# Kernel optimization log

Hardware: AMD Instinct MI355X
Metric: run time of the kernel (lower is better)

Reference implementation:

```python
import jax, jax.numpy as jnp
import numpy as np

BS, N_LINKS, MAX_LEN = 8192, 512, 32
D_LINK, D_PATH, D_READ, N_OUT = 32, 128, 256, 3
BN_EPS = 1e-5


def setup_inputs() -> dict:
    key = jax.random.key(0)
    ks = jax.random.split(key, 16)
    capa = jax.random.uniform(ks[0], (BS, N_LINKS), jnp.float32, 0.5, 1.0) * 100.0
    avail = jax.random.uniform(ks[1], (BS, N_LINKS), jnp.float32) * capa
    loss = jax.random.uniform(ks[2], (BS, N_LINKS), jnp.float32) * 0.05
    demand = jax.random.uniform(ks[3], (BS,), jnp.float32) * 10.0
    path = jax.random.randint(ks[4], (BS, MAX_LEN), 0, N_LINKS)
    hop_num = jax.random.randint(ks[5], (BS,), 1, MAX_LEN + 1)
    s = 0.1
    inp = {
        "demand": demand,
        "link_avail_capacity": avail,
        "link_capacity": capa,
        "link_loss": loss,
        "path": path,
        "hop_num": hop_num,
        # GRU params (PyTorch layout: [3H, D] gates ordered r,z,n)
        "gru_w_ih": jax.random.normal(ks[6], (3 * D_PATH, D_LINK), jnp.float32) * s,
        "gru_w_hh": jax.random.normal(ks[7], (3 * D_PATH, D_PATH), jnp.float32) * s,
        "gru_b_ih": jax.random.normal(ks[8], (3 * D_PATH,), jnp.float32) * s,
        "gru_b_hh": jax.random.normal(ks[9], (3 * D_PATH,), jnp.float32) * s,
        "bn_gamma": jnp.ones((D_PATH,), jnp.float32),
        "bn_beta": jnp.zeros((D_PATH,), jnp.float32),
        # stacked readout heads [N_OUT, ...]
        "rW1": jax.random.normal(ks[10], (N_OUT, D_PATH, D_READ), jnp.float32) * s,
        "rb1": jnp.zeros((N_OUT, D_READ), jnp.float32),
        "rW2": jax.random.normal(ks[11], (N_OUT, D_READ, D_READ), jnp.float32) * s,
        "rb2": jnp.zeros((N_OUT, D_READ), jnp.float32),
        "rW3": jax.random.normal(ks[12], (N_OUT, D_READ, 1), jnp.float32) * s,
        "rb3": jnp.zeros((N_OUT, 1), jnp.float32),
    }
    return inp


def _gru_scan(x_bt, h0, w_ih, w_hh, b_ih, b_hh):
    # x_bt: [B, T, D]; h0: [B, H] -> outputs [B, T, H]
    H = h0.shape[-1]
    def step(h, x_t):
        gi = x_t @ w_ih.T + b_ih          # [B, 3H]
        gh = h @ w_hh.T + b_hh            # [B, 3H]
        i_r, i_z, i_n = gi[:, :H], gi[:, H:2*H], gi[:, 2*H:]
        h_r, h_z, h_n = gh[:, :H], gh[:, H:2*H], gh[:, 2*H:]
        r = jax.nn.sigmoid(i_r + h_r)
        z = jax.nn.sigmoid(i_z + h_z)
        n = jnp.tanh(i_n + r * h_n)
        h_new = (1.0 - z) * n + z * h
        return h_new, h_new
    _, outs = jax.lax.scan(step, h0, jnp.swapaxes(x_bt, 0, 1))
    return jnp.swapaxes(outs, 0, 1)


def reference(demand, link_avail_capacity, link_capacity, link_loss, path, hop_num,
              gru_w_ih, gru_w_hh, gru_b_ih, gru_b_hh, bn_gamma, bn_beta,
              rW1, rb1, rW2, rb2, rW3, rb3):
    bs, n_links = link_capacity.shape
    max_len = path.shape[1]
    max_capa = jax.lax.stop_gradient(jnp.max(link_capacity))
    # link_state: [B, n_links, D_LINK]; first D_LINK-4 channels are zeros
    feats = jnp.stack([
        link_avail_capacity / max_capa,
        link_capacity / max_capa,
        link_avail_capacity / link_capacity,
        link_loss,
    ], axis=-1)
    link_state = jnp.concatenate(
        [jnp.zeros((bs, n_links, D_LINK - 4), feats.dtype), feats], axis=-1)
    link_state = jax.lax.stop_gradient(link_state)  # original detaches
    # initial hidden: zeros except last channel = demand/max_capa
    h0 = jnp.concatenate(
        [jnp.zeros((bs, D_PATH - 1), feats.dtype), (demand / max_capa)[:, None]], axis=-1)
    # fused gather of link states along each path, masked past hop_num
    gathered = jnp.take_along_axis(link_state, path[:, :, None], axis=1)  # [B, T, D]
    mask = (jnp.arange(max_len)[None, :] < hop_num[:, None])[:, :, None]
    link_inputs = gathered * mask.astype(gathered.dtype)
    outputs = _gru_scan(link_inputs, h0, gru_w_ih, gru_w_hh, gru_b_ih, gru_b_hh)
    # extract hidden state at last hop of each path
    idx = (hop_num - 1)[:, None, None]
    flow = jnp.take_along_axis(outputs, idx, axis=1)[:, 0, :]  # [B, H]
    # BatchNorm1d (training mode: batch statistics, biased variance)
    mean = jnp.mean(flow, axis=0)
    var = jnp.mean((flow - mean) ** 2, axis=0)
    flow = (flow - mean) * jax.lax.rsqrt(var + BN_EPS) * bn_gamma + bn_beta
    # readout heads: Linear -> SELU -> Linear -> SELU -> Linear
    h1 = jax.nn.selu(jnp.einsum('bh,uhr->ubr', flow, rW1) + rb1[:, None, :])
    h2 = jax.nn.selu(jnp.einsum('ubr,urs->ubs', h1, rW2) + rb2[:, None, :])
    y = jnp.einsum('ubs,uso->ubo', h2, rW3) + rb3[:, None, :]  # [U, B, 1]
    return jnp.transpose(y[:, :, 0], (1, 0))  # [B, U]
```

## Files before the change

kernel.cpp:

```cpp
#include <hip/hip_runtime.h>


#define BS 8192
#define NL 512
#define ML 32
#define DP 128
#define DR 256
#define NJOB 512

#define OFF_SUM    64
#define OFF_SSQ    192
#define OFF_CUR    576
#define OFF_PERM   640
#define OFF_WHH16  (OFF_PERM + BS)
#define OFF_W1     (OFF_WHH16 + 24576)
#define OFF_W2     (OFF_W1 + 49152)
#define OFF_FEATS  (OFF_W2 + 98304)
#define OFF_FLOW   (OFF_FEATS + BS*ML*4)

#define FEATS_BLOCKS 1024
#define MAX_BLOCKS   256
#define WPREP_BLOCKS 1344
#define SORT_BID     (FEATS_BLOCKS + MAX_BLOCKS + WPREP_BLOCKS)
#define PREP_GRID    (SORT_BID + 1)

typedef _Float16 f16x8 __attribute__((ext_vector_type(8)));
typedef float    f32x4 __attribute__((ext_vector_type(4)));

__device__ __forceinline__ float sigmoidf_(float x){ return 1.0f/(1.0f+__expf(-x)); }
__device__ __forceinline__ float tanhf_(float x){
  float t = __expf(-2.0f*fabsf(x));
  float r = (1.0f-t)/(1.0f+t);
  return copysignf(r, x);
}
__device__ __forceinline__ float seluf_(float x){
  const float sc = 1.0507009873554805f, al = 1.6732632423543772f;
  return x > 0.0f ? sc*x : sc*al*(__expf(x)-1.0f);
}

__global__ void prep_all(const int* __restrict__ path, const int* __restrict__ hop,
                         const float* __restrict__ avail, const float* __restrict__ capa,
                         const float* __restrict__ loss, const float* __restrict__ whh,
                         const float* __restrict__ rW1, const float* __restrict__ rW2,
                         float* ws){
  const int bid = blockIdx.x;
  const int tid = threadIdx.x;

  if (bid < FEATS_BLOCKS){
    int idx = bid*256 + tid;
    int b = idx >> 5, t = idx & 31;
    float4 f = make_float4(0.f, 0.f, 0.f, 0.f);
    if (t < hop[b]){
      int l = path[idx];
      float a = avail[b*NL + l];
      float c = capa [b*NL + l];
      f.x = a; f.y = c; f.z = a / c; f.w = loss[b*NL + l];
    }
    ((float4*)(ws + OFF_FEATS))[idx] = f;
  } else if (bid < FEATS_BLOCKS + MAX_BLOCKS){
    const float4* c4 = (const float4*)capa;
    const int n4 = BS*NL/4;
    float m = 0.0f;
    for (int i = (bid - FEATS_BLOCKS)*256 + tid; i < n4; i += MAX_BLOCKS*256){
      float4 v = c4[i];
      m = fmaxf(m, fmaxf(fmaxf(v.x, v.y), fmaxf(v.z, v.w)));
    }
    #pragma unroll
    for (int o = 32; o > 0; o >>= 1) m = fmaxf(m, __shfl_down(m, o, 64));
    if ((tid & 63) == 0) atomicMax((int*)ws, __float_as_int(m));
  } else if (bid < SORT_BID){
    _Float16* whh16 = (_Float16*)(ws + OFF_WHH16);
    _Float16* w1    = (_Float16*)(ws + OFF_W1);
    _Float16* w2    = (_Float16*)(ws + OFF_W2);
    int i = (bid - FEATS_BLOCKS - MAX_BLOCKS)*256 + tid;
    if (i < 49152){
      whh16[i] = (_Float16)whh[i];
    } else if (i < 147456){
      int j = i - 49152; int u = j >> 15; int rem = j & 32767; int n = rem >> 7; int k = rem & 127;
      w1[j] = (_Float16)rW1[u*32768 + k*256 + n];
    } else if (i < 344064){
      int j = i - 147456; int u = j >> 16; int rem = j & 65535; int n = rem >> 8; int k = rem & 255;
      w2[j] = (_Float16)rW2[u*65536 + k*256 + n];
    }
  } else {
    __shared__ int hist[32], start[32];
    for (int i = 64 + tid; i < 640; i += 256) ws[i] = 0.0f;
    if (tid < 32) hist[tid] = 0;
    __syncthreads();
    for (int b = tid; b < BS; b += 256) atomicAdd(&hist[32 - hop[b]], 1);
    __syncthreads();
    if (tid == 0){ int acc = 0; for (int i = 0; i < 32; ++i){ start[i] = acc; acc += hist[i]; } }
    __syncthreads();
    int* perm = (int*)ws + OFF_PERM;
    for (int b = tid; b < BS; b += 256){
      int pos = atomicAdd(&start[32 - hop[b]], 1);
      perm[pos] = b;
    }
  }
}

__launch_bounds__(512, 3)
__global__ void kgru(const float* __restrict__ demand, const int* __restrict__ hop,
                     const float* __restrict__ wih, const float* __restrict__ bih,
                     const float* __restrict__ bhh, float* __restrict__ ws,
                     float* __restrict__ flow){
  __shared__ _Float16 hHI[2][16*136];
  __shared__ _Float16 hLO[2][16*136];
  __shared__ int s_q;
  const int tid  = threadIdx.x;
  const int w    = tid >> 6;
  const int lane = tid & 63;
  const int lm   = lane & 15;
  const int qd   = lane >> 4;
  const int ch   = w*16 + lm;
  const float inv_maxc = 1.0f / ws[0];
  const int* perm = (const int*)ws + OFF_PERM;
  int* cursor = (int*)ws + OFF_CUR;
  const float* feats = ws + OFF_FEATS;
  const _Float16* whh16 = (const _Float16*)(ws + OFF_WHH16);

  f16x8 bf[3][4];
  #pragma unroll
  for (int g = 0; g < 3; ++g){
    const int n = 128*g + ch;
    #pragma unroll
    for (int kc = 0; kc < 4; ++kc)
      bf[g][kc] = *(const f16x8*)(whh16 + n*128 + kc*32 + qd*8);
  }

  float wihc[3][4];
  #pragma unroll
  for (int g = 0; g < 3; ++g){
    #pragma unroll
    for (int c = 0; c < 4; ++c)
      wihc[g][c] = wih[(128*g + ch)*32 + 28 + c];
    wihc[g][0] *= inv_maxc;
    wihc[g][1] *= inv_maxc;
  }
  const float bR  = bih[ch]     + bhh[ch];
  const float bZ  = bih[128+ch] + bhh[128+ch];
  const float bNI = bih[256+ch];
  const float bNH = bhh[256+ch];

  float ssum = 0.f, ssq = 0.f;

  for (;;){
    if (tid == 0) s_q = atomicAdd(cursor, 1);
    __syncthreads();
    const int q = s_q;
    if (q >= NJOB) break;

    int it[4], hp[4];
    #pragma unroll
    for (int r = 0; r < 4; ++r){
      it[r] = perm[q*16 + qd*4 + r];
      hp[r] = hop[it[r]];
    }
    int tmax = max(max(hp[0],hp[1]), max(hp[2],hp[3]));
    tmax = max(tmax, __shfl_xor(tmax, 16, 64));
    tmax = max(tmax, __shfl_xor(tmax, 32, 64));

    float hprev[4];
    #pragma unroll
    for (int r = 0; r < 4; ++r){
      float h0 = (ch == 127) ? demand[it[r]] * inv_maxc : 0.0f;
      hprev[r] = h0;
      const int m = qd*4 + r;
      _Float16 hi = (_Float16)h0;
      hHI[0][m*136 + ch] = hi;
      hLO[0][m*136 + ch] = (_Float16)(h0 - (float)hi);
    }
    __syncthreads();

    for (int t = 0; t < tmax; ++t){
      const int cur = t & 1, nxt = cur ^ 1;
      f32x4 ft[4];
      #pragma unroll
      for (int r = 0; r < 4; ++r)
        ft[r] = *(const f32x4*)(feats + (it[r]*ML + t)*4);

      f16x8 ahi[4], alo[4];
      #pragma unroll
      for (int kc = 0; kc < 4; ++kc){
        const int off = lm*136 + kc*32 + qd*8;
        ahi[kc] = *(const f16x8*)(&hHI[cur][off]);
        alo[kc] = *(const f16x8*)(&hLO[cur][off]);
      }

      f32x4 acc[3];
      #pragma unroll
      for (int g = 0; g < 3; ++g){
        f32x4 a = {0.f, 0.f, 0.f, 0.f};
        #pragma unroll
        for (int kc = 0; kc < 4; ++kc){
          a = __builtin_amdgcn_mfma_f32_16x16x32_f16(ahi[kc], bf[g][kc], a, 0, 0, 0);
          a = __builtin_amdgcn_mfma_f32_16x16x32_f16(alo[kc], bf[g][kc], a, 0, 0, 0);
        }
        acc[g] = a;
      }

      #pragma unroll
      for (int r = 0; r < 4; ++r){
        float f0 = ft[r][0], f1 = ft[r][1], f2 = ft[r][2], f3 = ft[r][3];
        float gr = fmaf(wihc[0][0],f0, fmaf(wihc[0][1],f1, fmaf(wihc[0][2],f2, wihc[0][3]*f3)));
        float gz = fmaf(wihc[1][0],f0, fmaf(wihc[1][1],f1, fmaf(wihc[1][2],f2, wihc[1][3]*f3)));
        float gn = fmaf(wihc[2][0],f0, fmaf(wihc[2][1],f1, fmaf(wihc[2][2],f2, wihc[2][3]*f3)));
        float rr = sigmoidf_(acc[0][r] + gr + bR);
        float zz = sigmoidf_(acc[1][r] + gz + bZ);
        float nn = tanhf_(gn + bNI + rr*(acc[2][r] + bNH));
        float hn = fmaf(zz, hprev[r] - nn, nn);
        if (t < hp[r]) hprev[r] = hn;
        const int m = qd*4 + r;
        _Float16 hi = (_Float16)hprev[r];
        hHI[nxt][m*136 + ch] = hi;
        hLO[nxt][m*136 + ch] = (_Float16)(hprev[r] - (float)hi);
      }
      __syncthreads();
    }

    #pragma unroll
    for (int r = 0; r < 4; ++r){
      float v = hprev[r];
      flow[it[r]*DP + ch] = v;
      ssum += v;
      ssq  = fmaf(v, v, ssq);
    }
    __syncthreads();
  }

  ssum += __shfl_xor(ssum, 16, 64);  ssum += __shfl_xor(ssum, 32, 64);
  ssq  += __shfl_xor(ssq,  16, 64);  ssq  += __shfl_xor(ssq,  32, 64);
  if (qd == 0){
    atomicAdd(&ws[OFF_SUM + ch], ssum);
    atomicAdd(&ws[OFF_SSQ + ch], ssq);
  }
}

__launch_bounds__(256, 2)
__global__ void kmlp(const float* __restrict__ flow, const float* __restrict__ ws,
                     const float* __restrict__ gamma, const float* __restrict__ beta,
                     const float* __restrict__ rb1, const float* __restrict__ rb2,
                     const float* __restrict__ rW3, const float* __restrict__ rb3,
                     float* __restrict__ out){
  __shared__ _Float16 x_lds[32*136];
  __shared__ _Float16 h1_lds[32*264];
  __shared__ float aa[DP], bb[DP];
  __shared__ float y_part[4][32];
  const int tid  = threadIdx.x;
  const int w    = tid >> 6;
  const int lane = tid & 63;
  const int lm   = lane & 15;
  const int qd   = lane >> 4;
  const int b0   = blockIdx.x * 32;
  const int u    = blockIdx.y;
  const _Float16* w1 = (const _Float16*)(ws + OFF_W1) + u*(DR*DP);
  const _Float16* w2 = (const _Float16*)(ws + OFF_W2) + u*(DR*DR);

  if (tid < DP){
    float m = ws[OFF_SUM + tid] * (1.0f/BS);
    float q = ws[OFF_SSQ + tid] * (1.0f/BS);
    float rstd = rsqrtf(q - m*m + 1e-5f);
    float a = rstd * gamma[tid];
    aa[tid] = a;
    bb[tid] = fmaf(-m, a, beta[tid]);
  }
  __syncthreads();

  for (int idx = tid; idx < 32*DP; idx += 256){
    int i = idx >> 7, h = idx & 127;
    x_lds[i*136 + h] = (_Float16)fmaf(flow[(b0 + i)*DP + h], aa[h], bb[h]);
  }
  __syncthreads();

  {
    f16x8 b1[4][4];
    float bias1[4];
    #pragma unroll
    for (int nt = 0; nt < 4; ++nt){
      const int n = (4*w + nt)*16 + lm;
      bias1[nt] = rb1[u*DR + n];
      #pragma unroll
      for (int kc = 0; kc < 4; ++kc)
        b1[nt][kc] = *(const f16x8*)(w1 + n*DP + kc*32 + qd*8);
    }
    for (int mt = 0; mt < 2; ++mt){
      f16x8 a[4];
      #pragma unroll
      for (int kc = 0; kc < 4; ++kc)
        a[kc] = *(const f16x8*)(&x_lds[(mt*16 + lm)*136 + kc*32 + qd*8]);
      #pragma unroll
      for (int nt = 0; nt < 4; ++nt){
        f32x4 acc = {bias1[nt], bias1[nt], bias1[nt], bias1[nt]};
        #pragma unroll
        for (int kc = 0; kc < 4; ++kc)
          acc = __builtin_amdgcn_mfma_f32_16x16x32_f16(a[kc], b1[nt][kc], acc, 0, 0, 0);
        const int n = (4*w + nt)*16 + lm;
        #pragma unroll
        for (int r = 0; r < 4; ++r)
          h1_lds[(mt*16 + qd*4 + r)*264 + n] = (_Float16)seluf_(acc[r]);
      }
    }
  }
  __syncthreads();

  {
    f16x8 b2[4][8];
    float bias2[4], w3l[4];
    #pragma unroll
    for (int nt = 0; nt < 4; ++nt){
      const int n = (4*w + nt)*16 + lm;
      bias2[nt] = rb2[u*DR + n];
      w3l[nt]   = rW3[u*DR + n];
      #pragma unroll
      for (int kc = 0; kc < 8; ++kc)
        b2[nt][kc] = *(const f16x8*)(w2 + n*DR + kc*32 + qd*8);
    }
    for (int mt = 0; mt < 2; ++mt){
      f16x8 a[8];
      #pragma unroll
      for (int kc = 0; kc < 8; ++kc)
        a[kc] = *(const f16x8*)(&h1_lds[(mt*16 + lm)*264 + kc*32 + qd*8]);
      f32x4 acc2[4];
      #pragma unroll
      for (int nt = 0; nt < 4; ++nt){
        f32x4 acc = {bias2[nt], bias2[nt], bias2[nt], bias2[nt]};
        #pragma unroll
        for (int kc = 0; kc < 8; ++kc)
          acc = __builtin_amdgcn_mfma_f32_16x16x32_f16(a[kc], b2[nt][kc], acc, 0, 0, 0);
        acc2[nt] = acc;
      }
      float p[4];
      #pragma unroll
      for (int r = 0; r < 4; ++r){
        p[r] = 0.f;
        #pragma unroll
        for (int nt = 0; nt < 4; ++nt)
          p[r] += seluf_(acc2[nt][r]) * w3l[nt];
      }
      #pragma unroll
      for (int r = 0; r < 4; ++r){
        p[r] += __shfl_xor(p[r], 1, 64);
        p[r] += __shfl_xor(p[r], 2, 64);
        p[r] += __shfl_xor(p[r], 4, 64);
        p[r] += __shfl_xor(p[r], 8, 64);
      }
      if (lm == 0){
        #pragma unroll
        for (int r = 0; r < 4; ++r)
          y_part[w][mt*16 + qd*4 + r] = p[r];
      }
    }
  }
  __syncthreads();
  if (tid < 32){
    float y = y_part[0][tid] + y_part[1][tid] + y_part[2][tid] + y_part[3][tid] + rb3[u];
    out[(b0 + tid)*3 + u] = y;
  }
}

extern "C" void kernel_launch(void* const* d_in, const int* in_sizes, int n_in,
                              void* d_out, int out_size, void* d_ws, size_t ws_size,
                              hipStream_t stream){
  const float* demand = (const float*)d_in[0];
  const float* avail  = (const float*)d_in[1];
  const float* capa   = (const float*)d_in[2];
  const float* loss   = (const float*)d_in[3];
  const int*   path   = (const int*)d_in[4];
  const int*   hop    = (const int*)d_in[5];
  const float* wih    = (const float*)d_in[6];
  const float* whh    = (const float*)d_in[7];
  const float* bih    = (const float*)d_in[8];
  const float* bhh    = (const float*)d_in[9];
  const float* gamma  = (const float*)d_in[10];
  const float* beta   = (const float*)d_in[11];
  const float* rW1    = (const float*)d_in[12];
  const float* rb1    = (const float*)d_in[13];
  const float* rW2    = (const float*)d_in[14];
  const float* rb2    = (const float*)d_in[15];
  const float* rW3    = (const float*)d_in[16];
  const float* rb3    = (const float*)d_in[17];
  float* ws  = (float*)d_ws;
  float* out = (float*)d_out;

  prep_all <<<PREP_GRID, 256, 0, stream>>>(path, hop, avail, capa, loss,
                                           whh, rW1, rW2, ws);
  kgru     <<<384, 512, 0, stream>>>(demand, hop, wih, bih, bhh, ws, ws + OFF_FLOW);
  kmlp     <<<dim3(BS/32, 3), 256, 0, stream>>>(ws + OFF_FLOW, ws, gamma, beta,
                                                rb1, rb2, rW3, rb3, out);
}
```

Baseline: 235.1 us.

## Fold GRU input projection into MFMA, use static job mapping, restructure MLP loops

The GRU kernel drops its persistent atomic job queue. It now launches one block per 16-path job, with a block-to-job mapping that pairs long and short paths. The 4-wide input feature projection is folded into an extra K-chunk of the recurrent MFMA: features are staged in LDS as hi/lo fp16 next to the hidden state, which replaces the per-step scalar FMAs and the per-lane feature loads. Occupancy hints are raised for both kernels, and the MLP loops are reordered so weight fragments load per output tile instead of all at once, lowering register pressure. The trade is extra MFMA work per step, a wider LDS stride, and the fp16 rounding of the input weights, which changes precision slightly.

```diff
diff --git a/kernel.cpp b/kernel.cpp
--- a/kernel.cpp
+++ b/kernel.cpp
@@ -7,6 +7,7 @@
 #define DP 128
 #define DR 256
 #define NJOB 512
+#define ST 172
 
 #define OFF_SUM    64
 #define OFF_SSQ    192
@@ -99,14 +100,13 @@
   }
 }
 
-__launch_bounds__(512, 3)
+__launch_bounds__(512, 4)
 __global__ void kgru(const float* __restrict__ demand, const int* __restrict__ hop,
                      const float* __restrict__ wih, const float* __restrict__ bih,
                      const float* __restrict__ bhh, float* __restrict__ ws,
                      float* __restrict__ flow){
-  __shared__ _Float16 hHI[2][16*136];
-  __shared__ _Float16 hLO[2][16*136];
-  __shared__ int s_q;
+  __shared__ _Float16 hHI[2][16*ST];
+  __shared__ _Float16 hLO[2][16*ST];
   const int tid  = threadIdx.x;
   const int w    = tid >> 6;
   const int lane = tid & 63;
@@ -115,119 +115,130 @@
   const int ch   = w*16 + lm;
   const float inv_maxc = 1.0f / ws[0];
   const int* perm = (const int*)ws + OFF_PERM;
-  int* cursor = (int*)ws + OFF_CUR;
   const float* feats = ws + OFF_FEATS;
   const _Float16* whh16 = (const _Float16*)(ws + OFF_WHH16);
 
-  f16x8 bf[3][4];
+  const int bid = blockIdx.x;
+  const int q = (bid < 256) ? bid : 767 - bid;
+
+  for (int idx = tid; idx < 1024; idx += 512){
+    const int buf = idx >> 9;
+    const int rem = idx & 511;
+    const int m   = rem >> 5;
+    const int c   = 128 + (rem & 31);
+    hHI[buf][m*ST + c] = (_Float16)0.f;
+    hLO[buf][m*ST + c] = (_Float16)0.f;
+  }
+
+  f16x8 bfr[5], bfz[5], bfnh[4], bfni;
   #pragma unroll
-  for (int g = 0; g < 3; ++g){
-    const int n = 128*g + ch;
-    #pragma unroll
-    for (int kc = 0; kc < 4; ++kc)
-      bf[g][kc] = *(const f16x8*)(whh16 + n*128 + kc*32 + qd*8);
-  }
-
-  float wihc[3][4];
-  #pragma unroll
-  for (int g = 0; g < 3; ++g){
-    #pragma unroll
-    for (int c = 0; c < 4; ++c)
-      wihc[g][c] = wih[(128*g + ch)*32 + 28 + c];
-    wihc[g][0] *= inv_maxc;
-    wihc[g][1] *= inv_maxc;
+  for (int kc = 0; kc < 4; ++kc){
+    bfr[kc]  = *(const f16x8*)(whh16 + (      ch)*128 + kc*32 + qd*8);
+    bfz[kc]  = *(const f16x8*)(whh16 + (128 + ch)*128 + kc*32 + qd*8);
+    bfnh[kc] = *(const f16x8*)(whh16 + (256 + ch)*128 + kc*32 + qd*8);
+  }
+  bfr[4] = (f16x8)0; bfz[4] = (f16x8)0; bfni = (f16x8)0;
+  if (qd == 0){
+    #pragma unroll
+    for (int j = 0; j < 4; ++j){
+      float s = (j < 2) ? inv_maxc : 1.0f;
+      bfr[4][j] = (_Float16)(wih[(      ch)*32 + 28 + j] * s);
+      bfz[4][j] = (_Float16)(wih[(128 + ch)*32 + 28 + j] * s);
+      bfni[j]   = (_Float16)(wih[(256 + ch)*32 + 28 + j] * s);
+    }
   }
   const float bR  = bih[ch]     + bhh[ch];
   const float bZ  = bih[128+ch] + bhh[128+ch];
   const float bNI = bih[256+ch];
   const float bNH = bhh[256+ch];
 
+  int it[4], hp[4];
+  #pragma unroll
+  for (int r = 0; r < 4; ++r){
+    it[r] = perm[q*16 + qd*4 + r];
+    hp[r] = hop[it[r]];
+  }
+  int tmax = max(max(hp[0],hp[1]), max(hp[2],hp[3]));
+  tmax = max(tmax, __shfl_xor(tmax, 16, 64));
+  tmax = max(tmax, __shfl_xor(tmax, 32, 64));
+
+  const int fw_i = w*2 + (lane >> 2);
+  const int fw_c = lane & 3;
+  const bool fw  = (lane < 8);
+  const int  fw_b = fw ? perm[q*16 + fw_i] : 0;
+
+  __syncthreads();
+
+  float hprev[4];
+  #pragma unroll
+  for (int r = 0; r < 4; ++r){
+    float h0 = (ch == 127) ? demand[it[r]] * inv_maxc : 0.0f;
+    hprev[r] = h0;
+    const int m = qd*4 + r;
+    _Float16 hi = (_Float16)h0;
+    hHI[0][m*ST + ch] = hi;
+    hLO[0][m*ST + ch] = (_Float16)(h0 - (float)hi);
+  }
+  if (fw){
+    float v = feats[(fw_b*ML + 0)*4 + fw_c];
+    _Float16 hi = (_Float16)v;
+    hHI[0][fw_i*ST + 128 + fw_c] = hi;
+    hLO[0][fw_i*ST + 128 + fw_c] = (_Float16)(v - (float)hi);
+  }
+  __syncthreads();
+
+  for (int t = 0; t < tmax; ++t){
+    const int cur = t & 1, nxt = cur ^ 1;
+    if (fw && (t+1) < ML){
+      float v = feats[(fw_b*ML + t + 1)*4 + fw_c];
+      _Float16 hi = (_Float16)v;
+      hHI[nxt][fw_i*ST + 128 + fw_c] = hi;
+      hLO[nxt][fw_i*ST + 128 + fw_c] = (_Float16)(v - (float)hi);
+    }
+
+    f32x4 accr = {0.f,0.f,0.f,0.f}, accz = {0.f,0.f,0.f,0.f};
+    f32x4 accnh = {0.f,0.f,0.f,0.f}, accni = {0.f,0.f,0.f,0.f};
+    #pragma unroll
+    for (int kc = 0; kc < 5; ++kc){
+      const int off = lm*ST + kc*32 + qd*8;
+      f16x8 ahi = *(const f16x8*)(&hHI[cur][off]);
+      f16x8 alo = *(const f16x8*)(&hLO[cur][off]);
+      accr = __builtin_amdgcn_mfma_f32_16x16x32_f16(ahi, bfr[kc], accr, 0, 0, 0);
+      accr = __builtin_amdgcn_mfma_f32_16x16x32_f16(alo, bfr[kc], accr, 0, 0, 0);
+      accz = __builtin_amdgcn_mfma_f32_16x16x32_f16(ahi, bfz[kc], accz, 0, 0, 0);
+      accz = __builtin_amdgcn_mfma_f32_16x16x32_f16(alo, bfz[kc], accz, 0, 0, 0);
+      if (kc < 4){
+        accnh = __builtin_amdgcn_mfma_f32_16x16x32_f16(ahi, bfnh[kc], accnh, 0, 0, 0);
+        accnh = __builtin_amdgcn_mfma_f32_16x16x32_f16(alo, bfnh[kc], accnh, 0, 0, 0);
+      } else {
+        accni = __builtin_amdgcn_mfma_f32_16x16x32_f16(ahi, bfni, accni, 0, 0, 0);
+        accni = __builtin_amdgcn_mfma_f32_16x16x32_f16(alo, bfni, accni, 0, 0, 0);
+      }
+    }
+
+    #pragma unroll
+    for (int r = 0; r < 4; ++r){
+      float rr = sigmoidf_(accr[r] + bR);
+      float zz = sigmoidf_(accz[r] + bZ);
+      float nn = tanhf_(accni[r] + bNI + rr*(accnh[r] + bNH));
+      float hn = fmaf(zz, hprev[r] - nn, nn);
+      if (t < hp[r]) hprev[r] = hn;
+      const int m = qd*4 + r;
+      _Float16 hi = (_Float16)hprev[r];
+      hHI[nxt][m*ST + ch] = hi;
+      hLO[nxt][m*ST + ch] = (_Float16)(hprev[r] - (float)hi);
+    }
+    __syncthreads();
+  }
+
   float ssum = 0.f, ssq = 0.f;
-
-  for (;;){
-    if (tid == 0) s_q = atomicAdd(cursor, 1);
-    __syncthreads();
-    const int q = s_q;
-    if (q >= NJOB) break;
-
-    int it[4], hp[4];
-    #pragma unroll
-    for (int r = 0; r < 4; ++r){
-      it[r] = perm[q*16 + qd*4 + r];
-      hp[r] = hop[it[r]];
-    }
-    int tmax = max(max(hp[0],hp[1]), max(hp[2],hp[3]));
-    tmax = max(tmax, __shfl_xor(tmax, 16, 64));
-    tmax = max(tmax, __shfl_xor(tmax, 32, 64));
-
-    float hprev[4];
-    #pragma unroll
-    for (int r = 0; r < 4; ++r){
-      float h0 = (ch == 127) ? demand[it[r]] * inv_maxc : 0.0f;
-      hprev[r] = h0;
-      const int m = qd*4 + r;
-      _Float16 hi = (_Float16)h0;
-      hHI[0][m*136 + ch] = hi;
-      hLO[0][m*136 + ch] = (_Float16)(h0 - (float)hi);
-    }
-    __syncthreads();
-
-    for (int t = 0; t < tmax; ++t){
-      const int cur = t & 1, nxt = cur ^ 1;
-      f32x4 ft[4];
-      #pragma unroll
-      for (int r = 0; r < 4; ++r)
-        ft[r] = *(const f32x4*)(feats + (it[r]*ML + t)*4);
-
-      f16x8 ahi[4], alo[4];
-      #pragma unroll
-      for (int kc = 0; kc < 4; ++kc){
-        const int off = lm*136 + kc*32 + qd*8;
-        ahi[kc] = *(const f16x8*)(&hHI[cur][off]);
-        alo[kc] = *(const f16x8*)(&hLO[cur][off]);
-      }
-
-      f32x4 acc[3];
-      #pragma unroll
-      for (int g = 0; g < 3; ++g){
-        f32x4 a = {0.f, 0.f, 0.f, 0.f};
-        #pragma unroll
-        for (int kc = 0; kc < 4; ++kc){
-          a = __builtin_amdgcn_mfma_f32_16x16x32_f16(ahi[kc], bf[g][kc], a, 0, 0, 0);
-          a = __builtin_amdgcn_mfma_f32_16x16x32_f16(alo[kc], bf[g][kc], a, 0, 0, 0);
-        }
-        acc[g] = a;
-      }
-
-      #pragma unroll
-      for (int r = 0; r < 4; ++r){
-        float f0 = ft[r][0], f1 = ft[r][1], f2 = ft[r][2], f3 = ft[r][3];
-        float gr = fmaf(wihc[0][0],f0, fmaf(wihc[0][1],f1, fmaf(wihc[0][2],f2, wihc[0][3]*f3)));
-        float gz = fmaf(wihc[1][0],f0, fmaf(wihc[1][1],f1, fmaf(wihc[1][2],f2, wihc[1][3]*f3)));
-        float gn = fmaf(wihc[2][0],f0, fmaf(wihc[2][1],f1, fmaf(wihc[2][2],f2, wihc[2][3]*f3)));
-        float rr = sigmoidf_(acc[0][r] + gr + bR);
-        float zz = sigmoidf_(acc[1][r] + gz + bZ);
-        float nn = tanhf_(gn + bNI + rr*(acc[2][r] + bNH));
-        float hn = fmaf(zz, hprev[r] - nn, nn);
-        if (t < hp[r]) hprev[r] = hn;
-        const int m = qd*4 + r;
-        _Float16 hi = (_Float16)hprev[r];
-        hHI[nxt][m*136 + ch] = hi;
-        hLO[nxt][m*136 + ch] = (_Float16)(hprev[r] - (float)hi);
-      }
-      __syncthreads();
-    }
-
-    #pragma unroll
-    for (int r = 0; r < 4; ++r){
-      float v = hprev[r];
-      flow[it[r]*DP + ch] = v;
-      ssum += v;
-      ssq  = fmaf(v, v, ssq);
-    }
-    __syncthreads();
-  }
-
+  #pragma unroll
+  for (int r = 0; r < 4; ++r){
+    float v = hprev[r];
+    flow[it[r]*DP + ch] = v;
+    ssum += v;
+    ssq  = fmaf(v, v, ssq);
+  }
   ssum += __shfl_xor(ssum, 16, 64);  ssum += __shfl_xor(ssum, 32, 64);
   ssq  += __shfl_xor(ssq,  16, 64);  ssq  += __shfl_xor(ssq,  32, 64);
   if (qd == 0){
@@ -236,7 +247,7 @@
   }
 }
 
-__launch_bounds__(256, 2)
+__launch_bounds__(256, 3)
 __global__ void kmlp(const float* __restrict__ flow, const float* __restrict__ ws,
                      const float* __restrict__ gamma, const float* __restrict__ beta,
                      const float* __restrict__ rb1, const float* __restrict__ rb2,
@@ -273,28 +284,25 @@
   __syncthreads();
 
   {
-    f16x8 b1[4][4];
-    float bias1[4];
-    #pragma unroll
+    f16x8 a1[2][4];
+    #pragma unroll
+    for (int mt = 0; mt < 2; ++mt)
+      #pragma unroll
+      for (int kc = 0; kc < 4; ++kc)
+        a1[mt][kc] = *(const f16x8*)(&x_lds[(mt*16 + lm)*136 + kc*32 + qd*8]);
     for (int nt = 0; nt < 4; ++nt){
       const int n = (4*w + nt)*16 + lm;
-      bias1[nt] = rb1[u*DR + n];
+      const float bias1 = rb1[u*DR + n];
+      f16x8 b1[4];
       #pragma unroll
       for (int kc = 0; kc < 4; ++kc)
-        b1[nt][kc] = *(const f16x8*)(w1 + n*DP + kc*32 + qd*8);
-    }
-    for (int mt = 0; mt < 2; ++mt){
-      f16x8 a[4];
-      #pragma unroll
-      for (int kc = 0; kc < 4; ++kc)
-        a[kc] = *(const f16x8*)(&x_lds[(mt*16 + lm)*136 + kc*32 + qd*8]);
-      #pragma unroll
-      for (int nt = 0; nt < 4; ++nt){
-        f32x4 acc = {bias1[nt], bias1[nt], bias1[nt], bias1[nt]};
+        b1[kc] = *(const f16x8*)(w1 + n*DP + kc*32 + qd*8);
+      #pragma unroll
+      for (int mt = 0; mt < 2; ++mt){
+        f32x4 acc = {bias1, bias1, bias1, bias1};
         #pragma unroll
         for (int kc = 0; kc < 4; ++kc)
-          acc = __builtin_amdgcn_mfma_f32_16x16x32_f16(a[kc], b1[nt][kc], acc, 0, 0, 0);
-        const int n = (4*w + nt)*16 + lm;
+          acc = __builtin_amdgcn_mfma_f32_16x16x32_f16(a1[mt][kc], b1[kc], acc, 0, 0, 0);
         #pragma unroll
         for (int r = 0; r < 4; ++r)
           h1_lds[(mt*16 + qd*4 + r)*264 + n] = (_Float16)seluf_(acc[r]);
@@ -304,50 +312,42 @@
   __syncthreads();
 
   {
-    f16x8 b2[4][8];
-    float bias2[4], w3l[4];
-    #pragma unroll
+    f16x8 a2[2][8];
+    #pragma unroll
+    for (int mt = 0; mt < 2; ++mt)
+      #pragma unroll
+      for (int kc = 0; kc < 8; ++kc)
+        a2[mt][kc] = *(const f16x8*)(&h1_lds[(mt*16 + lm)*264 + kc*32 + qd*8]);
+    float p[2][4] = {{0.f,0.f,0.f,0.f},{0.f,0.f,0.f,0.f}};
     for (int nt = 0; nt < 4; ++nt){
       const int n = (4*w + nt)*16 + lm;
-      bias2[nt] = rb2[u*DR + n];
-      w3l[nt]   = rW3[u*DR + n];
+      const float bias2 = rb2[u*DR + n];
+      const float w3l   = rW3[u*DR + n];
+      f16x8 b2[8];
       #pragma unroll
       for (int kc = 0; kc < 8; ++kc)
-        b2[nt][kc] = *(const f16x8*)(w2 + n*DR + kc*32 + qd*8);
-    }
-    for (int mt = 0; mt < 2; ++mt){
-      f16x8 a[8];
-      #pragma unroll
-      for (int kc = 0; kc < 8; ++kc)
-        a[kc] = *(const f16x8*)(&h1_lds[(mt*16 + lm)*264 + kc*32 + qd*8]);
-      f32x4 acc2[4];
-      #pragma unroll
-      for (int nt = 0; nt < 4; ++nt){
-        f32x4 acc = {bias2[nt], bias2[nt], bias2[nt], bias2[nt]};
+        b2[kc] = *(const f16x8*)(w2 + n*DR + kc*32 + qd*8);
+      #pragma unroll
+      for (int mt = 0; mt < 2; ++mt){
+        f32x4 acc = {bias2, bias2, bias2, bias2};
         #pragma unroll
         for (int kc = 0; kc < 8; ++kc)
-          acc = __builtin_amdgcn_mfma_f32_16x16x32_f16(a[kc], b2[nt][kc], acc, 0, 0, 0);
-        acc2[nt] = acc;
-      }
-      float p[4];
-      #pragma unroll
-      for (int r = 0; r < 4; ++r){
-        p[r] = 0.f;
-        #pragma unroll
-        for (int nt = 0; nt < 4; ++nt)
-          p[r] += seluf_(acc2[nt][r]) * w3l[nt];
-      }
-      #pragma unroll
-      for (int r = 0; r < 4; ++r){
-        p[r] += __shfl_xor(p[r], 1, 64);
-        p[r] += __shfl_xor(p[r], 2, 64);
-        p[r] += __shfl_xor(p[r], 4, 64);
-        p[r] += __shfl_xor(p[r], 8, 64);
-      }
-      if (lm == 0){
+          acc = __builtin_amdgcn_mfma_f32_16x16x32_f16(a2[mt][kc], b2[kc], acc, 0, 0, 0);
         #pragma unroll
         for (int r = 0; r < 4; ++r)
-          y_part[w][mt*16 + qd*4 + r] = p[r];
+          p[mt][r] += seluf_(acc[r]) * w3l;
+      }
+    }
+    #pragma unroll
+    for (int mt = 0; mt < 2; ++mt){
+      #pragma unroll
+      for (int r = 0; r < 4; ++r){
+        float v = p[mt][r];
+        v += __shfl_xor(v, 1, 64);
+        v += __shfl_xor(v, 2, 64);
+        v += __shfl_xor(v, 4, 64);
+        v += __shfl_xor(v, 8, 64);
+        if (lm == 0) y_part[w][mt*16 + qd*4 + r] = v;
       }
     }
   }
@@ -384,7 +384,7 @@
 
   prep_all <<<PREP_GRID, 256, 0, stream>>>(path, hop, avail, capa, loss,
                                            whh, rW1, rW2, ws);
-  kgru     <<<384, 512, 0, stream>>>(demand, hop, wih, bih, bhh, ws, ws + OFF_FLOW);
+  kgru     <<<NJOB, 512, 0, stream>>>(demand, hop, wih, bih, bhh, ws, ws + OFF_FLOW);
   kmlp     <<<dim3(BS/32, 3), 256, 0, stream>>>(ws + OFF_FLOW, ws, gamma, beta,
                                                 rb1, rb2, rW3, rb3, out);
 }
```

Measured after the change: 222.8 us. -5.3%, faster.
